# Kernel tuning notes

Measured on AMD Instinct MI355X. Metric: run time of the kernel, lower is better.

## Reference

```python
import jax, jax.numpy as jnp
import numpy as np
import math

SLIDING_WINDOW = 1024  # matches init kwarg

def setup_inputs() -> dict:
    key = jax.random.key(0)
    ks = jax.random.split(key, 6)
    B, S, Hq, Hkv, D = 1, 2048, 32, 8, 128
    NUM_PAGES, STRIDE = 300, 16
    q = jax.random.normal(ks[0], (B, S, Hq, D), dtype=jnp.float32)
    k = jax.random.normal(ks[1], (B, S, Hkv, D), dtype=jnp.float32)
    v = jax.random.normal(ks[2], (B, S, Hkv, D), dtype=jnp.float32)
    sink = jax.random.normal(ks[3], (Hq,), dtype=jnp.float32)
    cache_state = jnp.zeros((NUM_PAGES, STRIDE, 2, Hkv, D), dtype=jnp.float32)
    seq_block_ids = jax.random.randint(ks[4], (B, S // STRIDE), 0, NUM_PAGES, dtype=jnp.int64)
    return {"q": q, "k": k, "v": v, "sink": sink,
            "cache_state": cache_state, "seq_block_ids": seq_block_ids}


def reference(q, k, v, sink, cache_state, seq_block_ids):
    B, S, Hq, D = q.shape
    Hkv = k.shape[2]
    stride = cache_state.shape[1]

    # --- paged cache write (prefill side effect) ---
    kv = jnp.stack([k, v], axis=2)                       # [B,S,2,Hkv,D]
    pages = kv.reshape(B * (S // stride), stride, 2, Hkv, D)
    _ = cache_state.at[seq_block_ids.reshape(-1)].set(pages)

    # --- decomposed attention: matmul + mask + softmax(+sink) + matmul ---
    rep = Hq // Hkv
    ke = jnp.repeat(k, rep, axis=2)                      # [B,S,Hq,D] (GQA expand)
    ve = jnp.repeat(v, rep, axis=2)
    scale = 1.0 / math.sqrt(D)
    scores = jnp.einsum('bihd,bjhd->bhij', q, ke) * scale  # [B,Hq,S,S]

    i = jnp.arange(S)[:, None]
    j = jnp.arange(S)[None, :]
    allowed = (j <= i) & (i - j < SLIDING_WINDOW)        # causal + sliding window
    neg = jnp.finfo(scores.dtype).min
    logits = jnp.where(allowed, scores, neg)

    # attention sink: extra per-head logit appended; contributes to denominator only
    sink_l = jnp.broadcast_to(sink[None, :, None, None], (B, Hq, S, 1))
    probs = jax.nn.softmax(jnp.concatenate([logits, sink_l], axis=-1), axis=-1)[..., :S]

    out = jnp.einsum('bhij,bjhd->bihd', probs, ve)       # [B,S,Hq,D]
    return out
```

## Files before the change

kernel.cpp:

```cpp
#include <hip/hip_runtime.h>
#include <hip/hip_bf16.h>


#define S_LEN 2048
#define DH    128
#define HQ    32
#define HKV   8
#define WIN   1024
#define BR    64
#define BC    32
#define NT    (S_LEN / BC)
#define FM    16.0f
#define TILE_CH 512

typedef unsigned short u16;
typedef __attribute__((ext_vector_type(8))) short  short8;
typedef __attribute__((ext_vector_type(4))) float  floatx4;
typedef __attribute__((ext_vector_type(4))) unsigned int uintx4;

__device__ __forceinline__ unsigned rne1(float a) {
    unsigned u = __float_as_uint(a);
    return (u + 0x7FFFu + ((u >> 16) & 1u)) >> 16;
}
__device__ __forceinline__ unsigned rne_pk(float a, float b) {
    return rne1(a) | (rne1(b) << 16);
}
__device__ __forceinline__ unsigned cvt_pk(float a, float b) {
    unsigned r;
    asm("v_cvt_pk_bf16_f32 %0, %1, %2" : "=v"(r) : "v"(a), "v"(b));
    return r;
}

__global__ __launch_bounds__(256) void pack_kv(const float* __restrict__ kg,
                                               const float* __restrict__ vg,
                                               u16* __restrict__ kp,
                                               u16* __restrict__ vtp)
{
    __shared__ float Vs[BC][DH + 1];
    const int b   = blockIdx.x;
    const int hk  = b >> 6;
    const int jt  = b & 63;
    const int tid = threadIdx.x;
    const int j0  = jt * BC;

    #pragma unroll
    for (int t = 0; t < 4; t++) {
        int idx = tid + t * 256;
        int j   = idx >> 5;
        int dc  = idx & 31;
        floatx4 f = *(const floatx4*)(vg + ((size_t)(j0 + j) * HKV + hk) * DH + dc * 4);
        Vs[j][dc * 4 + 0] = f[0]; Vs[j][dc * 4 + 1] = f[1];
        Vs[j][dc * 4 + 2] = f[2]; Vs[j][dc * 4 + 3] = f[3];
    }

    u16* kpt = kp + (size_t)b * TILE_CH * 8;
    #pragma unroll
    for (int t = 0; t < 2; t++) {
        int c = tid + t * 256;
        int row = c >> 4, cc = c & 15;
        const float* p = kg + ((size_t)(j0 + row) * HKV + hk) * DH + cc * 8;
        floatx4 f0 = *(const floatx4*)p;
        floatx4 f1 = *(const floatx4*)(p + 4);
        int pc = (row << 4) | (cc ^ (row & 7));
        *(uintx4*)(kpt + pc * 8) =
            (uintx4){rne_pk(f0[0], f0[1]), rne_pk(f0[2], f0[3]),
                     rne_pk(f1[0], f1[1]), rne_pk(f1[2], f1[3])};
    }
    __syncthreads();

    u16* vpt = vtp + (size_t)b * TILE_CH * 8;
    #pragma unroll
    for (int t = 0; t < 2; t++) {
        int q  = tid + t * 256;
        int dd = q >> 2, c = q & 3;
        unsigned w0 = rne_pk(Vs[c * 4 + 0][dd], Vs[c * 4 + 16][dd]);
        unsigned w1 = rne_pk(Vs[c * 4 + 1][dd], Vs[c * 4 + 17][dd]);
        unsigned w2 = rne_pk(Vs[c * 4 + 2][dd], Vs[c * 4 + 18][dd]);
        unsigned w3 = rne_pk(Vs[c * 4 + 3][dd], Vs[c * 4 + 19][dd]);
        int qp = (dd << 2) | (c ^ ((dd >> 2) & 3));
        *(uintx4*)(vpt + qp * 8) = (uintx4){w0, w1, w2, w3};
    }
}

__launch_bounds__(128, 2)
__global__ void fa_kernel(const float* __restrict__ qg,
                          const u16* __restrict__ kp,
                          const u16* __restrict__ vtp,
                          const float* __restrict__ sg,
                          float* __restrict__ outg)
{
    __shared__ __align__(16) u16 Kt[2][TILE_CH * 8];
    __shared__ __align__(16) u16 Vt[2][TILE_CH * 8];
    __shared__ __align__(16) u16 Pb[BR * 40];

    const int tid  = threadIdx.x;
    const int w    = tid >> 6;
    const int lane = tid & 63;
    const int quad = lane >> 4;
    const int l16  = lane & 15;

    const int bid  = blockIdx.x;
    const int hk   = bid & 7;
    const int idx  = bid >> 3;
    const int hrem = idx & 3;
    const int u5   = (idx >> 2) & 7;
    const int t4   = idx >> 5;
    const int qbt[4] = {u5, 15 - u5, 16 + u5, 31 - u5};
    const int qb   = qbt[t4];
    const int h    = hk * 4 + hrem;

    const int i0 = qb * BR;
    const int m0 = i0 + w * 32;

    short8 qf[2][4];
    #pragma unroll
    for (int m = 0; m < 2; m++) {
        const float* qrow = qg + ((size_t)(m0 + m * 16 + l16) * HQ + h) * DH;
        #pragma unroll
        for (int kk = 0; kk < 4; kk++) {
            const float* p = qrow + kk * 32 + quad * 8;
            floatx4 f0 = *(const floatx4*)p;
            floatx4 f1 = *(const floatx4*)(p + 4);
            uintx4 u = (uintx4){cvt_pk(f0[0], f0[1]), cvt_pk(f0[2], f0[3]),
                                cvt_pk(f1[0], f1[1]), cvt_pk(f1[2], f1[3])};
            qf[m][kk] = *(short8*)&u;
        }
    }

    floatx4 acc[2][8];
    #pragma unroll
    for (int m = 0; m < 2; m++)
        #pragma unroll
        for (int i = 0; i < 8; i++) acc[m][i] = (floatx4){0.f, 0.f, 0.f, 0.f};
    float l_part[2][4] = {{0.f, 0.f, 0.f, 0.f}, {0.f, 0.f, 0.f, 0.f}};

    int c_r[2][4];
    #pragma unroll
    for (int m = 0; m < 2; m++)
        #pragma unroll
        for (int r = 0; r < 4; r++)
            c_r[m][r] = m0 + m * 16 + quad * 4 + r - l16;

    int jlo = i0 - (WIN - 1); if (jlo < 0) jlo = 0;
    const int jt_lo = jlo >> 5;
    const int jt_hi = (i0 + BR - 1) >> 5;

    const float SC2 = 0.08838834764831845f * 1.4426950408889634f;

    auto stage = [&](int bb, int jt) {
        const u16* kpt = kp  + ((size_t)(hk * NT + jt)) * TILE_CH * 8;
        const u16* vpt = vtp + ((size_t)(hk * NT + jt)) * TILE_CH * 8;
        #pragma unroll
        for (int it = 0; it < 4; it++) {
            int ch = tid + it * 128;
            __builtin_amdgcn_global_load_lds(
                (const __attribute__((address_space(1))) unsigned*)(kpt + ch * 8),
                (__attribute__((address_space(3))) unsigned*)(&Kt[bb][ch * 8]), 16, 0, 0);
            __builtin_amdgcn_global_load_lds(
                (const __attribute__((address_space(1))) unsigned*)(vpt + ch * 8),
                (__attribute__((address_space(3))) unsigned*)(&Vt[bb][ch * 8]), 16, 0, 0);
        }
    };

    stage(0, jt_lo);
    int bb = 0;

    for (int jt = jt_lo; jt <= jt_hi; jt++) {
        const int j0 = jt << 5;

        __syncthreads();

        if (jt < jt_hi) stage(bb ^ 1, jt + 1);

        floatx4 sc[2][2];
        #pragma unroll
        for (int m = 0; m < 2; m++) {
            sc[m][0] = (floatx4){0.f, 0.f, 0.f, 0.f};
            sc[m][1] = (floatx4){0.f, 0.f, 0.f, 0.f};
        }
        #pragma unroll
        for (int kk = 0; kk < 4; kk++) {
            const int cc = kk * 4 + quad;
            const int row0 = l16;
            const int row1 = 16 + l16;
            const int pc0 = (row0 << 4) | (cc ^ (row0 & 7));
            const int pc1 = (row1 << 4) | (cc ^ (row1 & 7));
            short8 kf0 = *(const short8*)(&Kt[bb][pc0 * 8]);
            short8 kf1 = *(const short8*)(&Kt[bb][pc1 * 8]);
            sc[0][0] = __builtin_amdgcn_mfma_f32_16x16x32_bf16(qf[0][kk], kf0, sc[0][0], 0, 0, 0);
            sc[1][0] = __builtin_amdgcn_mfma_f32_16x16x32_bf16(qf[1][kk], kf0, sc[1][0], 0, 0, 0);
            sc[0][1] = __builtin_amdgcn_mfma_f32_16x16x32_bf16(qf[0][kk], kf1, sc[0][1], 0, 0, 0);
            sc[1][1] = __builtin_amdgcn_mfma_f32_16x16x32_bf16(qf[1][kk], kf1, sc[1][1], 0, 0, 0);
        }

        const bool interior = (j0 + (BC - 1) <= i0) && (j0 >= i0 + BR - WIN);
        if (interior) {
            #pragma unroll
            for (int m = 0; m < 2; m++) {
                const int prow0 = w * 32 + m * 16 + quad * 4;
                #pragma unroll
                for (int r = 0; r < 4; r++) {
                    float p0 = exp2f(fmaf(sc[m][0][r], SC2, -FM));
                    float p1 = exp2f(fmaf(sc[m][1][r], SC2, -FM));
                    l_part[m][r] += p0 + p1;
                    *(unsigned*)(&Pb[(prow0 + r) * 40 + l16 * 2]) = cvt_pk(p0, p1);
                }
            }
        } else {
            #pragma unroll
            for (int m = 0; m < 2; m++) {
                const int prow0 = w * 32 + m * 16 + quad * 4;
                #pragma unroll
                for (int r = 0; r < 4; r++) {
                    bool a0 = (j0 <= c_r[m][r]) && (j0 > c_r[m][r] - WIN);
                    bool a1 = (j0 + 16 <= c_r[m][r]) && (j0 + 16 > c_r[m][r] - WIN);
                    float p0 = a0 ? exp2f(fmaf(sc[m][0][r], SC2, -FM)) : 0.f;
                    float p1 = a1 ? exp2f(fmaf(sc[m][1][r], SC2, -FM)) : 0.f;
                    l_part[m][r] += p0 + p1;
                    *(unsigned*)(&Pb[(prow0 + r) * 40 + l16 * 2]) = cvt_pk(p0, p1);
                }
            }
        }

        {
            short8 pf0 = *(const short8*)(&Pb[(w * 32 + l16) * 40 + quad * 8]);
            short8 pf1 = *(const short8*)(&Pb[(w * 32 + 16 + l16) * 40 + quad * 8]);
            #pragma unroll
            for (int nf = 0; nf < 8; nf++) {
                int dd = nf * 16 + l16;
                int qp = (dd << 2) | (quad ^ ((dd >> 2) & 3));
                short8 vf = *(const short8*)(&Vt[bb][qp * 8]);
                acc[0][nf] = __builtin_amdgcn_mfma_f32_16x16x32_bf16(pf0, vf, acc[0][nf], 0, 0, 0);
                acc[1][nf] = __builtin_amdgcn_mfma_f32_16x16x32_bf16(pf1, vf, acc[1][nf], 0, 0, 0);
            }
        }
        bb ^= 1;
    }

    const float sk2 = exp2f(fmaf(sg[h], 1.4426950408889634f, -FM));
    float inv[2][4];
    #pragma unroll
    for (int m = 0; m < 2; m++)
        #pragma unroll
        for (int r = 0; r < 4; r++) {
            float l = l_part[m][r];
            #pragma unroll
            for (int off = 1; off < 16; off <<= 1)
                l += __shfl_xor(l, off);
            inv[m][r] = 1.f / (l + sk2);
        }
    #pragma unroll
    for (int m = 0; m < 2; m++)
        #pragma unroll
        for (int nf = 0; nf < 8; nf++) {
            int d = nf * 16 + l16;
            #pragma unroll
            for (int r = 0; r < 4; r++) {
                int ig = m0 + m * 16 + quad * 4 + r;
                outg[((size_t)ig * HQ + h) * DH + d] = acc[m][nf][r] * inv[m][r];
            }
        }
}

__launch_bounds__(256, 4)
__global__ void fa_fallback(const float* __restrict__ qg,
                            const float* __restrict__ kg,
                            const float* __restrict__ vg,
                            const float* __restrict__ sg,
                            float* __restrict__ outg)
{
    __shared__ __align__(16) u16 Kt[BC * DH];
    __shared__ __align__(16) u16 Vt[DH * BC];
    __shared__ __align__(16) u16 Pb[BR * 40];

    const int tid  = threadIdx.x;
    const int w    = tid >> 6;
    const int lane = tid & 63;
    const int quad = lane >> 4;
    const int l16  = lane & 15;

    const int qb = blockIdx.x / HQ;
    const int h  = blockIdx.x % HQ;
    const int hk = h >> 2;
    const int i0 = qb * BR;
    const int m0 = i0 + w * 16;

    short8 qf[4];
    {
        const float* qrow = qg + ((size_t)(m0 + l16) * HQ + h) * DH;
        #pragma unroll
        for (int kk = 0; kk < 4; kk++) {
            const float* p = qrow + kk * 32 + quad * 8;
            floatx4 f0 = *(const floatx4*)p;
            floatx4 f1 = *(const floatx4*)(p + 4);
            uintx4 u = (uintx4){rne_pk(f0[0], f0[1]), rne_pk(f0[2], f0[3]),
                                rne_pk(f1[0], f1[1]), rne_pk(f1[2], f1[3])};
            qf[kk] = *(short8*)&u;
        }
    }

    floatx4 acc[8];
    #pragma unroll
    for (int i = 0; i < 8; i++) acc[i] = (floatx4){0.f, 0.f, 0.f, 0.f};
    float l_part[4] = {0.f, 0.f, 0.f, 0.f};

    int jlo = i0 - (WIN - 1); if (jlo < 0) jlo = 0;
    const int jt_lo = jlo >> 5;
    const int jt_hi = (i0 + BR - 1) >> 5;
    const float SC2 = 0.08838834764831845f * 1.4426950408889634f;

    for (int jt = jt_lo; jt <= jt_hi; jt++) {
        const int j0 = jt << 5;
        __syncthreads();
        #pragma unroll
        for (int it = 0; it < 2; it++) {
            int g   = tid + 256 * it;
            int row = g >> 4, cc = g & 15;
            int pc  = (row << 4) | (cc ^ (row & 7));
            const float* kpp = kg + ((size_t)(j0 + row) * HKV + hk) * DH + cc * 8;
            floatx4 f0 = *(const floatx4*)kpp;
            floatx4 f1 = *(const floatx4*)(kpp + 4);
            *(uintx4*)(&Kt[pc * 8]) =
                (uintx4){rne_pk(f0[0], f0[1]), rne_pk(f0[2], f0[3]),
                         rne_pk(f1[0], f1[1]), rne_pk(f1[2], f1[3])};
        }
        #pragma unroll
        for (int it = 0; it < 2; it++) {
            int g  = tid + 256 * it;
            int d  = g & 127, jc = g >> 7;
            const float* vp = vg + ((size_t)(j0 + jc * 8) * HKV + hk) * DH + d;
            float e0 = vp[0 * HKV * DH], e1 = vp[1 * HKV * DH];
            float e2 = vp[2 * HKV * DH], e3 = vp[3 * HKV * DH];
            float e4 = vp[4 * HKV * DH], e5 = vp[5 * HKV * DH];
            float e6 = vp[6 * HKV * DH], e7 = vp[7 * HKV * DH];
            int pc = (d << 2) | (jc ^ ((d >> 2) & 3));
            *(uintx4*)(&Vt[pc * 8]) =
                (uintx4){rne_pk(e0, e1), rne_pk(e2, e3), rne_pk(e4, e5), rne_pk(e6, e7)};
        }
        __syncthreads();

        floatx4 sc[2];
        sc[0] = (floatx4){0.f, 0.f, 0.f, 0.f};
        sc[1] = (floatx4){0.f, 0.f, 0.f, 0.f};
        #pragma unroll
        for (int kk = 0; kk < 4; kk++) {
            #pragma unroll
            for (int n = 0; n < 2; n++) {
                int row = n * 16 + l16;
                int cc  = kk * 4 + quad;
                int pc  = (row << 4) | (cc ^ (row & 7));
                short8 kf = *(const short8*)(&Kt[pc * 8]);
                sc[n] = __builtin_amdgcn_mfma_f32_16x16x32_bf16(qf[kk], kf, sc[n], 0, 0, 0);
            }
        }
        #pragma unroll
        for (int r = 0; r < 4; r++) {
            int   i_g = m0 + quad * 4 + r;
            int   jg0 = j0 + l16, jg1 = j0 + 16 + l16;
            bool  a0  = (jg0 <= i_g) && (i_g - jg0 < WIN);
            bool  a1  = (jg1 <= i_g) && (i_g - jg1 < WIN);
            float p0  = a0 ? exp2f(fmaf(sc[0][r], SC2, -FM)) : 0.f;
            float p1  = a1 ? exp2f(fmaf(sc[1][r], SC2, -FM)) : 0.f;
            l_part[r] += p0 + p1;
            int prow = w * 16 + quad * 4 + r;
            *(unsigned*)(&Pb[prow * 40 + 2 * l16]) = rne_pk(p0, p1);
        }
        {
            short8 pf = *(const short8*)(&Pb[(w * 16 + l16) * 40 + quad * 8]);
            #pragma unroll
            for (int nf = 0; nf < 8; nf++) {
                int dd = nf * 16 + l16;
                int qp = (dd << 2) | (quad ^ ((dd >> 2) & 3));
                short8 vf = *(const short8*)(&Vt[qp * 8]);
                acc[nf] = __builtin_amdgcn_mfma_f32_16x16x32_bf16(pf, vf, acc[nf], 0, 0, 0);
            }
        }
    }

    const float sk2 = exp2f(fmaf(sg[h], 1.4426950408889634f, -FM));
    float inv[4];
    #pragma unroll
    for (int r = 0; r < 4; r++) {
        float l = l_part[r];
        #pragma unroll
        for (int off = 1; off < 16; off <<= 1)
            l += __shfl_xor(l, off);
        inv[r] = 1.f / (l + sk2);
    }
    #pragma unroll
    for (int nf = 0; nf < 8; nf++) {
        int d = nf * 16 + l16;
        #pragma unroll
        for (int r = 0; r < 4; r++) {
            int ig = m0 + quad * 4 + r;
            outg[((size_t)ig * HQ + h) * DH + d] = acc[nf][r] * inv[r];
        }
    }
}

extern "C" void kernel_launch(void* const* d_in, const int* in_sizes, int n_in,
                              void* d_out, int out_size, void* d_ws, size_t ws_size,
                              hipStream_t stream) {
    const float* q  = (const float*)d_in[0];
    const float* k  = (const float*)d_in[1];
    const float* v  = (const float*)d_in[2];
    const float* sk = (const float*)d_in[3];
    float* out = (float*)d_out;

    const size_t tile_elems = (size_t)HKV * NT * TILE_CH * 8;
    const size_t need = 2 * tile_elems * sizeof(u16);

    if (ws_size >= need) {
        u16* kp  = (u16*)d_ws;
        u16* vtp = kp + tile_elems;
        pack_kv<<<dim3(HKV * NT), 256, 0, stream>>>(k, v, kp, vtp);
        fa_kernel<<<dim3((S_LEN / BR) * HQ), 128, 0, stream>>>(q, kp, vtp, sk, out);
    } else {
        fa_fallback<<<dim3((S_LEN / BR) * HQ), 256, 0, stream>>>(q, k, v, sk, out);
    }
}
```

Measured before the change: 170.2 us.

## Load K/V fragments directly from global into registers with per-wave balanced row groups

Drops the LDS double-buffered K/V staging and shared-memory barriers. Each wave now reads its K and V MFMA fragments straight from the pre-swizzled global tiles into registers, with K software-pipelined one tile ahead. Blocks become 256 threads where each of the 4 waves owns an independent 32-row query group chosen as {u, 31-u, 32+u, 63-u} to balance causal work. It also adds s_setprio around the MFMA bursts. Because waves in a block no longer share staged K/V, each wave issues its own global (L2) reads, which adds traffic and register pressure in exchange for removing the syncs.

Result: slower. 265.4 us (+55.9%).

```diff
diff --git a/kernel.cpp b/kernel.cpp
--- a/kernel.cpp
+++ b/kernel.cpp
@@ -7,7 +7,6 @@
 #define HQ    32
 #define HKV   8
 #define WIN   1024
-#define BR    64
 #define BC    32
 #define NT    (S_LEN / BC)
 #define FM    16.0f
@@ -82,16 +81,14 @@
     }
 }
 
-__launch_bounds__(128, 2)
+__launch_bounds__(256, 2)
 __global__ void fa_kernel(const float* __restrict__ qg,
                           const u16* __restrict__ kp,
                           const u16* __restrict__ vtp,
                           const float* __restrict__ sg,
                           float* __restrict__ outg)
 {
-    __shared__ __align__(16) u16 Kt[2][TILE_CH * 8];
-    __shared__ __align__(16) u16 Vt[2][TILE_CH * 8];
-    __shared__ __align__(16) u16 Pb[BR * 40];
+    __shared__ __align__(16) u16 Pb[4 * 32 * 40];
 
     const int tid  = threadIdx.x;
     const int w    = tid >> 6;
@@ -103,28 +100,40 @@
     const int hk   = bid & 7;
     const int idx  = bid >> 3;
     const int hrem = idx & 3;
-    const int u5   = (idx >> 2) & 7;
-    const int t4   = idx >> 5;
-    const int qbt[4] = {u5, 15 - u5, 16 + u5, 31 - u5};
-    const int qb   = qbt[t4];
+    const int u    = idx >> 2;
     const int h    = hk * 4 + hrem;
-
-    const int i0 = qb * BR;
-    const int m0 = i0 + w * 32;
+    const int rgt[4] = {u, 31 - u, 32 + u, 63 - u};
+    const int rg   = rgt[w];
+    const int i0w  = rg * 32;
 
     short8 qf[2][4];
     #pragma unroll
     for (int m = 0; m < 2; m++) {
-        const float* qrow = qg + ((size_t)(m0 + m * 16 + l16) * HQ + h) * DH;
+        const float* qrow = qg + ((size_t)(i0w + m * 16 + l16) * HQ + h) * DH;
         #pragma unroll
         for (int kk = 0; kk < 4; kk++) {
             const float* p = qrow + kk * 32 + quad * 8;
             floatx4 f0 = *(const floatx4*)p;
             floatx4 f1 = *(const floatx4*)(p + 4);
-            uintx4 u = (uintx4){cvt_pk(f0[0], f0[1]), cvt_pk(f0[2], f0[3]),
-                                cvt_pk(f1[0], f1[1]), cvt_pk(f1[2], f1[3])};
-            qf[m][kk] = *(short8*)&u;
-        }
+            uintx4 uq = (uintx4){cvt_pk(f0[0], f0[1]), cvt_pk(f0[2], f0[3]),
+                                 cvt_pk(f1[0], f1[1]), cvt_pk(f1[2], f1[3])};
+            qf[m][kk] = *(short8*)&uq;
+        }
+    }
+
+    int koff[8], voff[8];
+    #pragma unroll
+    for (int n = 0; n < 2; n++)
+        #pragma unroll
+        for (int kk = 0; kk < 4; kk++) {
+            int row = n * 16 + l16;
+            int cc  = kk * 4 + quad;
+            koff[n * 4 + kk] = ((row << 4) | (cc ^ (row & 7))) * 8;
+        }
+    #pragma unroll
+    for (int nf = 0; nf < 8; nf++) {
+        int dd = nf * 16 + l16;
+        voff[nf] = ((dd << 2) | (quad ^ ((dd >> 2) & 3))) * 8;
     }
 
     floatx4 acc[2][8];
@@ -139,61 +148,48 @@
     for (int m = 0; m < 2; m++)
         #pragma unroll
         for (int r = 0; r < 4; r++)
-            c_r[m][r] = m0 + m * 16 + quad * 4 + r - l16;
-
-    int jlo = i0 - (WIN - 1); if (jlo < 0) jlo = 0;
+            c_r[m][r] = i0w + m * 16 + quad * 4 + r - l16;
+
+    int jlo = i0w - (WIN - 1); if (jlo < 0) jlo = 0;
     const int jt_lo = jlo >> 5;
-    const int jt_hi = (i0 + BR - 1) >> 5;
+    const int jt_hi = rg;
 
     const float SC2 = 0.08838834764831845f * 1.4426950408889634f;
 
-    auto stage = [&](int bb, int jt) {
-        const u16* kpt = kp  + ((size_t)(hk * NT + jt)) * TILE_CH * 8;
-        const u16* vpt = vtp + ((size_t)(hk * NT + jt)) * TILE_CH * 8;
-        #pragma unroll
-        for (int it = 0; it < 4; it++) {
-            int ch = tid + it * 128;
-            __builtin_amdgcn_global_load_lds(
-                (const __attribute__((address_space(1))) unsigned*)(kpt + ch * 8),
-                (__attribute__((address_space(3))) unsigned*)(&Kt[bb][ch * 8]), 16, 0, 0);
-            __builtin_amdgcn_global_load_lds(
-                (const __attribute__((address_space(1))) unsigned*)(vpt + ch * 8),
-                (__attribute__((address_space(3))) unsigned*)(&Vt[bb][ch * 8]), 16, 0, 0);
-        }
+    const u16* kbase = kp  + (((size_t)hk * NT) << 12);
+    const u16* vbase = vtp + (((size_t)hk * NT) << 12);
+
+    short8 kfA[8], kfB[8], vf[8];
+
+    auto loadK = [&](short8 (&kf)[8], int jtt) {
+        const u16* t = kbase + ((size_t)jtt << 12);
+        #pragma unroll
+        for (int i = 0; i < 8; i++) kf[i] = *(const short8*)(t + koff[i]);
     };
-
-    stage(0, jt_lo);
-    int bb = 0;
-
-    for (int jt = jt_lo; jt <= jt_hi; jt++) {
-        const int j0 = jt << 5;
-
-        __syncthreads();
-
-        if (jt < jt_hi) stage(bb ^ 1, jt + 1);
-
+    auto loadV = [&](int jtt) {
+        const u16* t = vbase + ((size_t)jtt << 12);
+        #pragma unroll
+        for (int i = 0; i < 8; i++) vf[i] = *(const short8*)(t + voff[i]);
+    };
+
+    auto compute = [&](int j0, short8 (&kf)[8]) {
         floatx4 sc[2][2];
         #pragma unroll
         for (int m = 0; m < 2; m++) {
             sc[m][0] = (floatx4){0.f, 0.f, 0.f, 0.f};
             sc[m][1] = (floatx4){0.f, 0.f, 0.f, 0.f};
         }
+        __builtin_amdgcn_s_setprio(1);
         #pragma unroll
         for (int kk = 0; kk < 4; kk++) {
-            const int cc = kk * 4 + quad;
-            const int row0 = l16;
-            const int row1 = 16 + l16;
-            const int pc0 = (row0 << 4) | (cc ^ (row0 & 7));
-            const int pc1 = (row1 << 4) | (cc ^ (row1 & 7));
-            short8 kf0 = *(const short8*)(&Kt[bb][pc0 * 8]);
-            short8 kf1 = *(const short8*)(&Kt[bb][pc1 * 8]);
-            sc[0][0] = __builtin_amdgcn_mfma_f32_16x16x32_bf16(qf[0][kk], kf0, sc[0][0], 0, 0, 0);
-            sc[1][0] = __builtin_amdgcn_mfma_f32_16x16x32_bf16(qf[1][kk], kf0, sc[1][0], 0, 0, 0);
-            sc[0][1] = __builtin_amdgcn_mfma_f32_16x16x32_bf16(qf[0][kk], kf1, sc[0][1], 0, 0, 0);
-            sc[1][1] = __builtin_amdgcn_mfma_f32_16x16x32_bf16(qf[1][kk], kf1, sc[1][1], 0, 0, 0);
-        }
-
-        const bool interior = (j0 + (BC - 1) <= i0) && (j0 >= i0 + BR - WIN);
+            sc[0][0] = __builtin_amdgcn_mfma_f32_16x16x32_bf16(qf[0][kk], kf[kk],     sc[0][0], 0, 0, 0);
+            sc[1][0] = __builtin_amdgcn_mfma_f32_16x16x32_bf16(qf[1][kk], kf[kk],     sc[1][0], 0, 0, 0);
+            sc[0][1] = __builtin_amdgcn_mfma_f32_16x16x32_bf16(qf[0][kk], kf[4 + kk], sc[0][1], 0, 0, 0);
+            sc[1][1] = __builtin_amdgcn_mfma_f32_16x16x32_bf16(qf[1][kk], kf[4 + kk], sc[1][1], 0, 0, 0);
+        }
+        __builtin_amdgcn_s_setprio(0);
+
+        const bool interior = (j0 + (BC - 1) <= i0w) && (j0 >= i0w + 32 - WIN);
         if (interior) {
             #pragma unroll
             for (int m = 0; m < 2; m++) {
@@ -222,19 +218,29 @@
             }
         }
 
-        {
-            short8 pf0 = *(const short8*)(&Pb[(w * 32 + l16) * 40 + quad * 8]);
-            short8 pf1 = *(const short8*)(&Pb[(w * 32 + 16 + l16) * 40 + quad * 8]);
-            #pragma unroll
-            for (int nf = 0; nf < 8; nf++) {
-                int dd = nf * 16 + l16;
-                int qp = (dd << 2) | (quad ^ ((dd >> 2) & 3));
-                short8 vf = *(const short8*)(&Vt[bb][qp * 8]);
-                acc[0][nf] = __builtin_amdgcn_mfma_f32_16x16x32_bf16(pf0, vf, acc[0][nf], 0, 0, 0);
-                acc[1][nf] = __builtin_amdgcn_mfma_f32_16x16x32_bf16(pf1, vf, acc[1][nf], 0, 0, 0);
-            }
-        }
-        bb ^= 1;
+        short8 pf0 = *(const short8*)(&Pb[(w * 32 + l16) * 40 + quad * 8]);
+        short8 pf1 = *(const short8*)(&Pb[(w * 32 + 16 + l16) * 40 + quad * 8]);
+        __builtin_amdgcn_s_setprio(1);
+        #pragma unroll
+        for (int nf = 0; nf < 8; nf++) {
+            acc[0][nf] = __builtin_amdgcn_mfma_f32_16x16x32_bf16(pf0, vf[nf], acc[0][nf], 0, 0, 0);
+            acc[1][nf] = __builtin_amdgcn_mfma_f32_16x16x32_bf16(pf1, vf[nf], acc[1][nf], 0, 0, 0);
+        }
+        __builtin_amdgcn_s_setprio(0);
+    };
+
+    int jt = jt_lo;
+    loadK(kfA, jt);
+    for (;;) {
+        loadV(jt);
+        if (jt < jt_hi) loadK(kfB, jt + 1);
+        compute(jt << 5, kfA);
+        if (++jt > jt_hi) break;
+
+        loadV(jt);
+        if (jt < jt_hi) loadK(kfA, jt + 1);
+        compute(jt << 5, kfB);
+        if (++jt > jt_hi) break;
     }
 
     const float sk2 = exp2f(fmaf(sg[h], 1.4426950408889634f, -FM));
@@ -256,7 +262,7 @@
             int d = nf * 16 + l16;
             #pragma unroll
             for (int r = 0; r < 4; r++) {
-                int ig = m0 + m * 16 + quad * 4 + r;
+                int ig = i0w + m * 16 + quad * 4 + r;
                 outg[((size_t)ig * HQ + h) * DH + d] = acc[m][nf][r] * inv[m][r];
             }
         }
@@ -271,7 +277,7 @@
 {
     __shared__ __align__(16) u16 Kt[BC * DH];
     __shared__ __align__(16) u16 Vt[DH * BC];
-    __shared__ __align__(16) u16 Pb[BR * 40];
+    __shared__ __align__(16) u16 Pb[64 * 40];
 
     const int tid  = threadIdx.x;
     const int w    = tid >> 6;
@@ -282,7 +288,7 @@
     const int qb = blockIdx.x / HQ;
     const int h  = blockIdx.x % HQ;
     const int hk = h >> 2;
-    const int i0 = qb * BR;
+    const int i0 = qb * 64;
     const int m0 = i0 + w * 16;
 
     short8 qf[4];
@@ -306,7 +312,7 @@
 
     int jlo = i0 - (WIN - 1); if (jlo < 0) jlo = 0;
     const int jt_lo = jlo >> 5;
-    const int jt_hi = (i0 + BR - 1) >> 5;
+    const int jt_hi = (i0 + 63) >> 5;
     const float SC2 = 0.08838834764831845f * 1.4426950408889634f;
 
     for (int jt = jt_lo; jt <= jt_hi; jt++) {
@@ -414,8 +420,8 @@
         u16* kp  = (u16*)d_ws;
         u16* vtp = kp + tile_elems;
         pack_kv<<<dim3(HKV * NT), 256, 0, stream>>>(k, v, kp, vtp);
-        fa_kernel<<<dim3((S_LEN / BR) * HQ), 128, 0, stream>>>(q, kp, vtp, sk, out);
+        fa_kernel<<<dim3(512), 256, 0, stream>>>(q, kp, vtp, sk, out);
     } else {
-        fa_fallback<<<dim3((S_LEN / BR) * HQ), 256, 0, stream>>>(q, k, v, sk, out);
-    }
-}
+        fa_fallback<<<dim3((S_LEN / 64) * HQ), 256, 0, stream>>>(q, k, v, sk, out);
+    }
+}
```
